# Kernel optimization log

Hardware: AMD Instinct MI355X
Metric: run time of the kernel (lower is better)

Reference implementation:

```python
import jax, jax.numpy as jnp
import numpy as np

NUM_HEADS = 16
HIDDEN = 1024
EPS = 1e-5


def _layer_norm(x, g, b):
    m = jnp.mean(x, axis=-1, keepdims=True)
    v = jnp.mean(jnp.square(x - m), axis=-1, keepdims=True)
    return (x - m) * jax.lax.rsqrt(v + EPS) * g + b


def setup_inputs() -> dict:
    key = jax.random.key(0)
    ks = jax.random.split(key, 6)
    B, S, H = 2, 2048, HIDDEN
    x = jax.random.normal(ks[0], (B, S, H), dtype=jnp.float32)
    # True = masked (original passes ~attn_mask to SDPA); causal mask
    causal = ~jnp.tril(jnp.ones((S, S), dtype=bool))
    attn_mask = causal[None, None, :, :]  # [1,1,S,S]
    sc = 1.0 / np.sqrt(H)
    qkv_w = jax.random.normal(ks[1], (H, 3 * H), dtype=jnp.float32) * sc
    qkv_b = jnp.zeros((3 * H,), dtype=jnp.float32)
    out_w = jax.random.normal(ks[2], (H, H), dtype=jnp.float32) * sc
    out_b = jnp.zeros((H,), dtype=jnp.float32)
    w1 = jax.random.normal(ks[3], (H, 4 * H), dtype=jnp.float32) * sc
    b1 = jnp.zeros((4 * H,), dtype=jnp.float32)
    w2 = jax.random.normal(ks[4], (4 * H, H), dtype=jnp.float32) * (1.0 / np.sqrt(4 * H))
    b2 = jnp.zeros((H,), dtype=jnp.float32)
    return {
        'x': x, 'attn_mask': attn_mask,
        'qkv_w': qkv_w, 'qkv_b': qkv_b, 'out_w': out_w, 'out_b': out_b,
        'w1': w1, 'b1': b1, 'w2': w2, 'b2': b2,
        'ln1_g': jnp.ones((H,), jnp.float32), 'ln1_b': jnp.zeros((H,), jnp.float32),
        'ln2_g': jnp.ones((H,), jnp.float32), 'ln2_b': jnp.zeros((H,), jnp.float32),
    }


def reference(x, attn_mask, qkv_w, qkv_b, out_w, out_b, w1, b1, w2, b2,
              ln1_g, ln1_b, ln2_g, ln2_b):
    B, S, H = x.shape
    nh = NUM_HEADS
    hd = H // nh
    qkv = x @ qkv_w + qkv_b                      # [B,S,3H]
    q, k, v = jnp.split(qkv, 3, axis=-1)
    q = q.reshape(B, S, nh, hd).transpose(0, 2, 1, 3)  # [B,nh,S,hd]
    k = k.reshape(B, S, nh, hd).transpose(0, 2, 1, 3)
    v = v.reshape(B, S, nh, hd).transpose(0, 2, 1, 3)
    scores = jnp.einsum('bhqd,bhkd->bhqk', q, k) / jnp.sqrt(jnp.asarray(hd, x.dtype))
    scores = jnp.where(attn_mask, jnp.finfo(scores.dtype).min, scores)
    p = jax.nn.softmax(scores, axis=-1)
    attn = jnp.einsum('bhqk,bhkd->bhqd', p, v)   # [B,nh,S,hd]
    attn = attn.transpose(0, 2, 1, 3).reshape(B, S, H)
    attn = attn @ out_w + out_b
    x = _layer_norm(x + attn, ln1_g, ln1_b)
    h = jax.nn.relu(x @ w1 + b1) @ w2 + b2
    x = _layer_norm(x + h, ln2_g, ln2_b)
    return x
```

## Files before the change

kernel.cpp:

```cpp
#include <hip/hip_runtime.h>
#include <hip/hip_bf16.h>

typedef __bf16 bf16x8 __attribute__((ext_vector_type(8)));
typedef __bf16 bf16x4 __attribute__((ext_vector_type(4)));
typedef float f32x4 __attribute__((ext_vector_type(4)));

__device__ __forceinline__ void gload16(void* lds, const void* g) {
  __builtin_amdgcn_global_load_lds((const __attribute__((address_space(1))) void*)g,
                                   (__attribute__((address_space(3))) void*)lds, 16, 0, 0);
}

__global__ __launch_bounds__(256)
void transpose_cast(const float* __restrict__ in, __bf16* __restrict__ out, int R, int C)
{
  __shared__ __bf16 tile[32][33];
  const int bc = blockIdx.x * 32, br = blockIdx.y * 32;
  const int lx = threadIdx.x & 31, ly = threadIdx.x >> 5;
#pragma unroll
  for (int p = 0; p < 4; ++p)
    tile[ly + p * 8][lx] = (__bf16)in[(size_t)(br + ly + p * 8) * C + bc + lx];
  __syncthreads();
#pragma unroll
  for (int p = 0; p < 4; ++p)
    out[(size_t)(bc + ly + p * 8) * R + br + lx] = tile[lx][ly + p * 8];
}

__global__ __launch_bounds__(256)
void vtrans(const __bf16* __restrict__ qkv, __bf16* __restrict__ vtg)
{
  __shared__ __bf16 tile[32][33];
  const int sx = blockIdx.x * 32;
  const int dy = blockIdx.y * 32;
  const int z = blockIdx.z;
  const int b = z >> 4, h = z & 15;
  const int lx = threadIdx.x & 31, ly = threadIdx.x >> 5;
  const __bf16* src = qkv + (size_t)b * 2048 * 3072 + 2048 + h * 64;
#pragma unroll
  for (int p = 0; p < 4; ++p)
    tile[ly + p * 8][lx] = src[(size_t)(sx + ly + p * 8) * 3072 + dy + lx];
  __syncthreads();
  __bf16* dst = vtg + (size_t)z * 64 * 2048;
#pragma unroll
  for (int p = 0; p < 4; ++p)
    dst[(size_t)(dy + ly + p * 8) * 2048 + sx + lx] = tile[lx][ly + p * 8];
}

__global__ __launch_bounds__(256)
void cast_bf16(const float* __restrict__ in, __bf16* __restrict__ out)
{
  const int i = (blockIdx.x * 256 + threadIdx.x) * 4;
  float4 v = *(const float4*)(in + i);
  out[i] = (__bf16)v.x; out[i + 1] = (__bf16)v.y;
  out[i + 2] = (__bf16)v.z; out[i + 3] = (__bf16)v.w;
}

template<int BN, bool OUT_BF16, bool RELU, bool RESID>
__global__ __launch_bounds__(256)
void gemm_bt(const __bf16* __restrict__ A, const __bf16* __restrict__ Bt,
             const float* __restrict__ bias, const float* __restrict__ resid,
             void* __restrict__ Cv, int M, int N, int K)
{
  constexpr int NW = BN / 32;
  __shared__ __bf16 As[2][128 * 64];
  __shared__ __bf16 Bs[2][BN * 64];
  const int tid = threadIdx.x;
  const int wave = tid >> 6, lane = tid & 63;
  const int g = lane >> 4, l16 = lane & 15;
  const int row0 = blockIdx.x * 128, col0 = blockIdx.y * BN;
  const int wr = wave >> 1, wc = wave & 1;
  f32x4 acc[4][NW] = {};
  const int nk = K >> 6;

  auto STAGE = [&](int buf, int k0) {
#pragma unroll
    for (int r = 0; r < 4; ++r) {
      const int seg = r * 256 + tid;
      const int arow = seg >> 3;
      const int ko = ((seg & 7) ^ (arow & 7)) * 8;
      gload16(&As[buf][(r * 256 + wave * 64) * 8], &A[(size_t)(row0 + arow) * K + k0 + ko]);
    }
#pragma unroll
    for (int r = 0; r < BN / 32; ++r) {
      const int seg = r * 256 + tid;
      const int brow = seg >> 3;
      const int ko = ((seg & 7) ^ (brow & 7)) * 8;
      gload16(&Bs[buf][(r * 256 + wave * 64) * 8], &Bt[(size_t)(col0 + brow) * K + k0 + ko]);
    }
  };

  STAGE(0, 0);
  __syncthreads();
  int cur = 0;
  for (int t = 0; t < nk; ++t) {
    if (t + 1 < nk) STAGE(cur ^ 1, (t + 1) << 6);
#pragma unroll
    for (int kk = 0; kk < 2; ++kk) {
      bf16x8 af[4], bfr[NW];
#pragma unroll
      for (int m = 0; m < 4; ++m) {
        const int row = wr * 64 + m * 16 + l16;
        af[m] = *(const bf16x8*)&As[cur][row * 64 + ((kk * 32 + g * 8) ^ ((row & 7) << 3))];
      }
#pragma unroll
      for (int n = 0; n < NW; ++n) {
        const int row = wc * (BN / 2) + n * 16 + l16;
        bfr[n] = *(const bf16x8*)&Bs[cur][row * 64 + ((kk * 32 + g * 8) ^ ((row & 7) << 3))];
      }
#pragma unroll
      for (int m = 0; m < 4; ++m)
#pragma unroll
        for (int n = 0; n < NW; ++n)
          acc[m][n] = __builtin_amdgcn_mfma_f32_16x16x32_bf16(af[m], bfr[n], acc[m][n], 0, 0, 0);
    }
    __syncthreads();
    cur ^= 1;
  }
#pragma unroll
  for (int n = 0; n < NW; ++n) {
    const int col = col0 + wc * (BN / 2) + n * 16 + l16;
    const float bv = bias[col];
#pragma unroll
    for (int m = 0; m < 4; ++m) {
      const int rrow = row0 + wr * 64 + m * 16 + g * 4;
#pragma unroll
      for (int r = 0; r < 4; ++r) {
        float v = acc[m][n][r] + bv;
        if (RESID) v += resid[(size_t)(rrow + r) * N + col];
        if (RELU)  v = fmaxf(v, 0.f);
        if (OUT_BF16) ((__bf16*)Cv)[(size_t)(rrow + r) * N + col] = (__bf16)v;
        else          ((float*)Cv)[(size_t)(rrow + r) * N + col] = v;
      }
    }
  }
}

template<bool RESID>
__global__ __launch_bounds__(256)
void gemm_splitk(const __bf16* __restrict__ A, const __bf16* __restrict__ Bt,
                 const float* __restrict__ bias, const float* __restrict__ resid,
                 float* __restrict__ C0, float* __restrict__ C1,
                 int M, int N, int Kfull, int Ksub)
{
  __shared__ __bf16 As[2][128 * 64];
  __shared__ __bf16 Bs[2][128 * 64];
  const int tid = threadIdx.x;
  const int wave = tid >> 6, lane = tid & 63;
  const int g = lane >> 4, l16 = lane & 15;
  const int row0 = blockIdx.x * 128, col0 = blockIdx.y * 128;
  const int z = blockIdx.z;
  const __bf16* Az = A + (size_t)z * Ksub;
  const __bf16* Bz = Bt + (size_t)z * Ksub;
  float* C = z ? C1 : C0;
  const int wr = wave >> 1, wc = wave & 1;
  f32x4 acc[4][4] = {};
  const int nk = Ksub >> 6;

  auto STAGE = [&](int buf, int k0) {
#pragma unroll
    for (int r = 0; r < 4; ++r) {
      const int seg = r * 256 + tid;
      const int arow = seg >> 3;
      const int ko = ((seg & 7) ^ (arow & 7)) * 8;
      gload16(&As[buf][(r * 256 + wave * 64) * 8], &Az[(size_t)(row0 + arow) * Kfull + k0 + ko]);
      gload16(&Bs[buf][(r * 256 + wave * 64) * 8], &Bz[(size_t)(col0 + arow) * Kfull + k0 + ko]);
    }
  };

  STAGE(0, 0);
  __syncthreads();
  int cur = 0;
  for (int t = 0; t < nk; ++t) {
    if (t + 1 < nk) STAGE(cur ^ 1, (t + 1) << 6);
#pragma unroll
    for (int kk = 0; kk < 2; ++kk) {
      bf16x8 af[4], bfr[4];
#pragma unroll
      for (int m = 0; m < 4; ++m) {
        const int row = wr * 64 + m * 16 + l16;
        af[m] = *(const bf16x8*)&As[cur][row * 64 + ((kk * 32 + g * 8) ^ ((row & 7) << 3))];
      }
#pragma unroll
      for (int n = 0; n < 4; ++n) {
        const int row = wc * 64 + n * 16 + l16;
        bfr[n] = *(const bf16x8*)&Bs[cur][row * 64 + ((kk * 32 + g * 8) ^ ((row & 7) << 3))];
      }
#pragma unroll
      for (int m = 0; m < 4; ++m)
#pragma unroll
        for (int n = 0; n < 4; ++n)
          acc[m][n] = __builtin_amdgcn_mfma_f32_16x16x32_bf16(af[m], bfr[n], acc[m][n], 0, 0, 0);
    }
    __syncthreads();
    cur ^= 1;
  }
#pragma unroll
  for (int n = 0; n < 4; ++n) {
    const int col = col0 + wc * 64 + n * 16 + l16;
    const float bv = (z == 0) ? bias[col] : 0.f;
#pragma unroll
    for (int m = 0; m < 4; ++m) {
      const int rrow = row0 + wr * 64 + m * 16 + g * 4;
#pragma unroll
      for (int r = 0; r < 4; ++r) {
        float v = acc[m][n][r] + bv;
        if (RESID) { if (z == 0) v += resid[(size_t)(rrow + r) * N + col]; }
        C[(size_t)(rrow + r) * N + col] = v;
      }
    }
  }
}

__global__ __launch_bounds__(256)
void attn_fwd(const __bf16* __restrict__ qkv, const __bf16* __restrict__ vtg,
              __bf16* __restrict__ ctx)
{
  constexpr int S = 2048, H = 1024, W3 = 3 * H;
  __shared__ __bf16 Ks[2][64 * 64];
  __shared__ __bf16 Vt[2][64 * 64];
  __shared__ __bf16 Ps[4][16 * 64];
  const int tid = threadIdx.x, wave = tid >> 6, lane = tid & 63;
  const int g = lane >> 4, l16 = lane & 15;
  const int perm = ((l16 & 7) << 1) | (l16 >> 3);
  const int bh = blockIdx.x;
  const int pr = blockIdx.y;
  const int b = bh >> 4, h = bh & 15;
  const size_t base = (size_t)b * S * W3;
  const __bf16* Qg = qkv + base;
  const __bf16* Kg = qkv + base + H;
  const __bf16* Vg = vtg + (size_t)bh * 64 * S;

  auto STAGE_KV = [&](int buf, int kv0) {
#pragma unroll
    for (int r = 0; r < 2; ++r) {
      const int seg = r * 256 + tid;
      const int row = seg >> 3;
      const int ko = ((seg & 7) ^ (row & 7)) * 8;
      gload16(&Ks[buf][(r * 256 + wave * 64) * 8], &Kg[(size_t)(kv0 + row) * W3 + h * 64 + ko]);
      gload16(&Vt[buf][(r * 256 + wave * 64) * 8], &Vg[(size_t)row * S + kv0 + ko]);
    }
  };

#pragma unroll 1
  for (int half = 0; half < 2; ++half) {
    const int qi = half ? (31 - blockIdx.y) : blockIdx.y;
    const int q0 = qi * 64;
    const int qrow = q0 + wave * 16 + l16;
    bf16x8 qa[2];
#pragma unroll
    for (int kk = 0; kk < 2; ++kk)
      qa[kk] = *(const bf16x8*)&Qg[(size_t)qrow * W3 + h * 64 + kk * 32 + g * 8];

    f32x4 o[4] = {};
    float lsum = 0.f;
    const int nT = qi + 1;

    STAGE_KV(0, 0);
    __syncthreads();
    int cur = 0;

    for (int t = 0; t < nT; ++t) {
      const int kv0 = t * 64;
      if (t + 1 < nT) STAGE_KV(cur ^ 1, kv0 + 64);

      f32x4 s[4] = {};
      __builtin_amdgcn_s_setprio(1);
#pragma unroll
      for (int kk = 0; kk < 2; ++kk) {
        bf16x8 kb[4];
#pragma unroll
        for (int n = 0; n < 4; ++n) {
          const int row = n * 16 + l16;
          kb[n] = *(const bf16x8*)&Ks[cur][row * 64 + ((kk * 32 + g * 8) ^ ((row & 7) << 3))];
        }
#pragma unroll
        for (int n = 0; n < 4; ++n)
          s[n] = __builtin_amdgcn_mfma_f32_16x16x32_bf16(kb[n], qa[kk], s[n], 0, 0, 0);
      }
      __builtin_amdgcn_s_setprio(0);

      const bool diag = (t == nT - 1);
#pragma unroll
      for (int n = 0; n < 4; ++n) {
        float lp[4];
#pragma unroll
        for (int r = 0; r < 4; ++r) {
          const int ka = kv0 + n * 16 + g * 4 + r;
          float p = exp2f(s[n][r] * 0.18033688f);
          if (diag && ka > qrow) p = 0.f;
          lp[r] = p;
          lsum += p;
        }
        bf16x4 pk;
        pk[0] = (__bf16)lp[0]; pk[1] = (__bf16)lp[1];
        pk[2] = (__bf16)lp[2]; pk[3] = (__bf16)lp[3];
        *(bf16x4*)&Ps[wave][l16 * 64 + (((4 * n + g) ^ perm) << 2)] = pk;
      }

      __builtin_amdgcn_s_setprio(1);
#pragma unroll
      for (int kk = 0; kk < 2; ++kk) {
        const int hb = 8 * kk + 2 * g;
        bf16x4 p0 = *(const bf16x4*)&Ps[wave][l16 * 64 + ((hb ^ perm) << 2)];
        bf16x4 p1 = *(const bf16x4*)&Ps[wave][l16 * 64 + (((hb + 1) ^ perm) << 2)];
        bf16x8 pa = __builtin_shufflevector(p0, p1, 0, 1, 2, 3, 4, 5, 6, 7);
        bf16x8 vb[4];
#pragma unroll
        for (int n2 = 0; n2 < 4; ++n2) {
          const int row = n2 * 16 + l16;
          vb[n2] = *(const bf16x8*)&Vt[cur][row * 64 + ((kk * 32 + g * 8) ^ ((row & 7) << 3))];
        }
#pragma unroll
        for (int n2 = 0; n2 < 4; ++n2)
          o[n2] = __builtin_amdgcn_mfma_f32_16x16x32_bf16(pa, vb[n2], o[n2], 0, 0, 0);
      }
      __builtin_amdgcn_s_setprio(0);
      __syncthreads();
      cur ^= 1;
    }

    lsum += __shfl_xor(lsum, 16);
    lsum += __shfl_xor(lsum, 32);
#pragma unroll
    for (int r = 0; r < 4; ++r) {
      const float den = __shfl(lsum, g * 4 + r);
      const float inv = 1.f / den;
      const int qr = q0 + wave * 16 + g * 4 + r;
#pragma unroll
      for (int n2 = 0; n2 < 4; ++n2) {
        const int d = n2 * 16 + l16;
        ctx[(size_t)(b * S + qr) * H + h * 64 + d] = (__bf16)(o[n2][r] * inv);
      }
    }
  }
}

template<bool WRITE_BF16, bool TWO_IN>
__global__ __launch_bounds__(256)
void ln_kernel(const float* __restrict__ in, const float* __restrict__ in2,
               const float* __restrict__ gw, const float* __restrict__ bw,
               float* __restrict__ outf, __bf16* __restrict__ outb)
{
  const int row = blockIdx.x, tid = threadIdx.x;
  float4 xv = ((const float4*)(in + (size_t)row * 1024))[tid];
  if (TWO_IN) {
    const float4 yv = ((const float4*)(in2 + (size_t)row * 1024))[tid];
    xv.x += yv.x; xv.y += yv.y; xv.z += yv.z; xv.w += yv.w;
  }
  float s = xv.x + xv.y + xv.z + xv.w;
  float s2 = xv.x * xv.x + xv.y * xv.y + xv.z * xv.z + xv.w * xv.w;
#pragma unroll
  for (int off = 32; off; off >>= 1) { s += __shfl_xor(s, off); s2 += __shfl_xor(s2, off); }
  __shared__ float ps[8];
  if ((tid & 63) == 0) { ps[tid >> 6] = s; ps[4 + (tid >> 6)] = s2; }
  __syncthreads();
  s = ps[0] + ps[1] + ps[2] + ps[3];
  s2 = ps[4] + ps[5] + ps[6] + ps[7];
  const float mean = s * (1.f / 1024.f);
  const float var = s2 * (1.f / 1024.f) - mean * mean;
  const float rs = rsqrtf(var + 1e-5f);
  const float4 gv = ((const float4*)gw)[tid];
  const float4 bv = ((const float4*)bw)[tid];
  float4 y;
  y.x = (xv.x - mean) * rs * gv.x + bv.x;
  y.y = (xv.y - mean) * rs * gv.y + bv.y;
  y.z = (xv.z - mean) * rs * gv.z + bv.z;
  y.w = (xv.w - mean) * rs * gv.w + bv.w;
  ((float4*)(outf + (size_t)row * 1024))[tid] = y;
  if (WRITE_BF16) {
    __bf16* ob = outb + (size_t)row * 1024 + tid * 4;
    ob[0] = (__bf16)y.x; ob[1] = (__bf16)y.y; ob[2] = (__bf16)y.z; ob[3] = (__bf16)y.w;
  }
}

extern "C" void kernel_launch(void* const* d_in, const int* in_sizes, int n_in,
                              void* d_out, int out_size, void* d_ws, size_t ws_size,
                              hipStream_t stream)
{
  (void)in_sizes; (void)n_in; (void)out_size; (void)ws_size;
  const float* x     = (const float*)d_in[0];
  const float* qkv_w = (const float*)d_in[2];
  const float* qkv_b = (const float*)d_in[3];
  const float* out_w = (const float*)d_in[4];
  const float* out_b = (const float*)d_in[5];
  const float* w1    = (const float*)d_in[6];
  const float* b1    = (const float*)d_in[7];
  const float* w2    = (const float*)d_in[8];
  const float* b2    = (const float*)d_in[9];
  const float* ln1g  = (const float*)d_in[10];
  const float* ln1b  = (const float*)d_in[11];
  const float* ln2g  = (const float*)d_in[12];
  const float* ln2b  = (const float*)d_in[13];

  char* ws = (char*)d_ws;
  __bf16* wt_qkv = (__bf16*)(ws + 0);
  __bf16* wt_out = (__bf16*)(ws + 6291456);
  __bf16* wt_w1  = (__bf16*)(ws + 8388608);
  __bf16* wt_w2  = (__bf16*)(ws + 16777216);
  __bf16* xb     = (__bf16*)(ws + 25165824);
  __bf16* big    = (__bf16*)(ws + 33554432);
  float*  res    = (float*)(ws + 67108864);
  float*  x1f    = (float*)(ws + 83886080);
  __bf16* x1b    = (__bf16*)(ws + 100663296);
  __bf16* vtg    = (__bf16*)res;
  float*  pB     = (float*)big;
  float*  qB     = (float*)ws;

  transpose_cast<<<dim3(96, 32), 256, 0, stream>>>(qkv_w, wt_qkv, 1024, 3072);
  transpose_cast<<<dim3(32, 32), 256, 0, stream>>>(out_w, wt_out, 1024, 1024);
  transpose_cast<<<dim3(128, 32), 256, 0, stream>>>(w1, wt_w1, 1024, 4096);
  transpose_cast<<<dim3(32, 128), 256, 0, stream>>>(w2, wt_w2, 4096, 1024);
  cast_bf16<<<4096, 256, 0, stream>>>(x, xb);

  gemm_bt<128, true, false, false><<<dim3(32, 24), 256, 0, stream>>>(xb, wt_qkv, qkv_b, nullptr, big, 4096, 3072, 1024);
  vtrans<<<dim3(64, 2, 32), 256, 0, stream>>>(big, vtg);
  attn_fwd<<<dim3(32, 16), 256, 0, stream>>>(big, vtg, xb);
  gemm_splitk<true><<<dim3(32, 8, 2), 256, 0, stream>>>(xb, wt_out, out_b, x, res, pB, 4096, 1024, 1024, 512);
  ln_kernel<true, true><<<4096, 256, 0, stream>>>(res, pB, ln1g, ln1b, x1f, x1b);
  gemm_bt<128, true, true, false><<<dim3(32, 32), 256, 0, stream>>>(x1b, wt_w1, b1, nullptr, big, 4096, 4096, 1024);
  gemm_splitk<true><<<dim3(32, 8, 2), 256, 0, stream>>>(big, wt_w2, b2, x1f, res, qB, 4096, 1024, 4096, 2048);
  ln_kernel<false, true><<<4096, 256, 0, stream>>>(res, qB, ln2g, ln2b, (float*)d_out, nullptr);
}
```

Baseline: 246.7 us.

## Add 256x256 eight-wave GEMM with interleaved prefetch and 4-way split-K FFN2

Introduces a 512-thread GEMM with 256x256 tiles that interleaves LDS staging of the next K-tiles with MFMA quarters, and uses it for the QKV and FFN1 projections. The FFN down projection becomes a 4-way split-K whose partials go into scratch buffers and are summed in a new fused four-input LayerNorm kernel. The out-projection switches from split-K to a single-pass gemm_bt with a fused residual. The aim is more data reuse per tile and better overlap of loads with compute. The cost is heavier register and LDS pressure and extra partial-sum traffic through reused workspace regions.

```diff
diff --git a/kernel.cpp b/kernel.cpp
--- a/kernel.cpp
+++ b/kernel.cpp
@@ -52,6 +52,151 @@
   float4 v = *(const float4*)(in + i);
   out[i] = (__bf16)v.x; out[i + 1] = (__bf16)v.y;
   out[i + 2] = (__bf16)v.z; out[i + 3] = (__bf16)v.w;
+}
+
+template<bool OUTBF16, bool RELU, bool SPLIT>
+__global__ __launch_bounds__(512, 2)
+void gemm256(const __bf16* __restrict__ A, const __bf16* __restrict__ Bt,
+             const float* __restrict__ bias,
+             void* __restrict__ C0v, float* __restrict__ P1,
+             float* __restrict__ P2lo, float* __restrict__ P2hi,
+             float* __restrict__ P3,
+             int M, int N, int Kfull, int Ksub)
+{
+  __shared__ __align__(16) __bf16 As[2][2][128 * 64];
+  __shared__ __align__(16) __bf16 Bs[2][2][128 * 64];
+  const int tid = threadIdx.x, wave = tid >> 6, lane = tid & 63;
+  const int g = lane >> 4, l16 = lane & 15;
+  const int wr = wave >> 2, wc = wave & 3;
+  const int row0 = blockIdx.x * 256, col0 = blockIdx.y * 256;
+  const int z = SPLIT ? blockIdx.z : 0;
+  const __bf16* Az = A + (size_t)z * Ksub;
+  const __bf16* Bz = Bt + (size_t)z * Ksub;
+  const int nk = Ksub >> 6;
+  f32x4 acc[8][4] = {};
+
+  auto SA = [&](int buf, int half, int kt) {
+    const int k0 = kt << 6;
+#pragma unroll
+    for (int r = 0; r < 2; ++r) {
+      const int seg = r * 512 + tid, rr = seg >> 3;
+      const int src = ((seg & 7) ^ (rr & 7)) << 3;
+      gload16(&As[buf][half][(size_t)(r * 512 + wave * 64) * 8],
+              &Az[(size_t)(row0 + half * 128 + rr) * Kfull + k0 + src]);
+    }
+  };
+  auto SB = [&](int buf, int half, int kt) {
+    const int k0 = kt << 6;
+#pragma unroll
+    for (int r = 0; r < 2; ++r) {
+      const int seg = r * 512 + tid, rr = seg >> 3;
+      const int src = ((seg & 7) ^ (rr & 7)) << 3;
+      gload16(&Bs[buf][half][(size_t)(r * 512 + wave * 64) * 8],
+              &Bz[(size_t)(col0 + half * 128 + rr) * Kfull + k0 + src]);
+    }
+  };
+
+  SA(0, 0, 0); SA(0, 1, 0); SB(0, 0, 0); SB(0, 1, 0);
+  { const int t1 = (nk > 1) ? 1 : 0; SB(1, 0, t1); SB(1, 1, t1); }
+  asm volatile("s_waitcnt vmcnt(4)" ::: "memory");
+  __builtin_amdgcn_sched_barrier(0);
+  __builtin_amdgcn_s_barrier();
+
+#pragma unroll 1
+  for (int t = 0; t < nk; ++t) {
+    const int p = t & 1;
+    const int tA = (t + 1 < nk) ? (t + 1) : (nk - 1);
+    const int tB = (t + 2 < nk) ? (t + 2) : (nk - 1);
+
+    bf16x8 bfr[4][2], af[2][2];
+
+#pragma unroll
+    for (int n = 0; n < 4; ++n) {
+      const int row = wc * 64 + n * 16 + l16;
+      const int hf = row >> 7, rr = row & 127;
+#pragma unroll
+      for (int ks = 0; ks < 2; ++ks)
+        bfr[n][ks] = *(const bf16x8*)&Bs[p][hf][rr * 64 + ((((ks << 2) + g) ^ (rr & 7)) << 3)];
+    }
+#pragma unroll
+    for (int m = 0; m < 2; ++m) {
+      const int rr = m * 16 + l16;
+#pragma unroll
+      for (int ks = 0; ks < 2; ++ks)
+        af[m][ks] = *(const bf16x8*)&As[p][wr][rr * 64 + ((((ks << 2) + g) ^ (rr & 7)) << 3)];
+    }
+    SA(p ^ 1, 0, tA);
+    __builtin_amdgcn_s_barrier();
+    asm volatile("s_waitcnt lgkmcnt(0)" ::: "memory");
+    __builtin_amdgcn_sched_barrier(0);
+    __builtin_amdgcn_s_setprio(1);
+#pragma unroll
+    for (int ks = 0; ks < 2; ++ks)
+#pragma unroll
+      for (int m = 0; m < 2; ++m)
+#pragma unroll
+        for (int n = 0; n < 4; ++n)
+          acc[m][n] = __builtin_amdgcn_mfma_f32_16x16x32_bf16(af[m][ks], bfr[n][ks], acc[m][n], 0, 0, 0);
+    __builtin_amdgcn_s_setprio(0);
+    __builtin_amdgcn_s_barrier();
+
+#pragma unroll
+    for (int q = 1; q < 4; ++q) {
+#pragma unroll
+      for (int m = 0; m < 2; ++m) {
+        const int rr = (2 * q + m) * 16 + l16;
+#pragma unroll
+        for (int ks = 0; ks < 2; ++ks)
+          af[m][ks] = *(const bf16x8*)&As[p][wr][rr * 64 + ((((ks << 2) + g) ^ (rr & 7)) << 3)];
+      }
+      if (q == 1)      SA(p ^ 1, 1, tA);
+      else if (q == 2) SB(p, 0, tB);
+      else             SB(p, 1, tB);
+      __builtin_amdgcn_s_barrier();
+      asm volatile("s_waitcnt lgkmcnt(0)" ::: "memory");
+      __builtin_amdgcn_sched_barrier(0);
+      __builtin_amdgcn_s_setprio(1);
+#pragma unroll
+      for (int ks = 0; ks < 2; ++ks)
+#pragma unroll
+        for (int m = 0; m < 2; ++m)
+#pragma unroll
+          for (int n = 0; n < 4; ++n)
+            acc[2 * q + m][n] = __builtin_amdgcn_mfma_f32_16x16x32_bf16(af[m][ks], bfr[n][ks], acc[2 * q + m][n], 0, 0, 0);
+      __builtin_amdgcn_s_setprio(0);
+      if (q == 3) {
+        asm volatile("s_waitcnt vmcnt(4)" ::: "memory");
+        __builtin_amdgcn_sched_barrier(0);
+      }
+      __builtin_amdgcn_s_barrier();
+    }
+  }
+
+#pragma unroll
+  for (int n = 0; n < 4; ++n) {
+    const int col = col0 + wc * 64 + n * 16 + l16;
+    float bv = 0.f;
+    if (!SPLIT || z == 0) bv = bias[col];
+#pragma unroll
+    for (int m = 0; m < 8; ++m) {
+      const int rbase = row0 + wr * 128 + m * 16 + g * 4;
+#pragma unroll
+      for (int j = 0; j < 4; ++j) {
+        float v = acc[m][n][j] + bv;
+        const size_t idx = (size_t)(rbase + j) * N + col;
+        if (SPLIT) {
+          if (z == 0)      ((float*)C0v)[idx] = v;
+          else if (z == 1) P1[idx] = v;
+          else if (z == 2) { float* C = (row0 < 2048) ? P2lo : P2hi; C[idx] = v; }
+          else             { v += P3[idx]; P3[idx] = v; }
+        } else {
+          if (RELU) v = fmaxf(v, 0.f);
+          if (OUTBF16) ((__bf16*)C0v)[idx] = (__bf16)v;
+          else         ((float*)C0v)[idx] = v;
+        }
+      }
+    }
+  }
 }
 
 template<int BN, bool OUT_BF16, bool RELU, bool RESID>
@@ -134,82 +279,6 @@
   }
 }
 
-template<bool RESID>
-__global__ __launch_bounds__(256)
-void gemm_splitk(const __bf16* __restrict__ A, const __bf16* __restrict__ Bt,
-                 const float* __restrict__ bias, const float* __restrict__ resid,
-                 float* __restrict__ C0, float* __restrict__ C1,
-                 int M, int N, int Kfull, int Ksub)
-{
-  __shared__ __bf16 As[2][128 * 64];
-  __shared__ __bf16 Bs[2][128 * 64];
-  const int tid = threadIdx.x;
-  const int wave = tid >> 6, lane = tid & 63;
-  const int g = lane >> 4, l16 = lane & 15;
-  const int row0 = blockIdx.x * 128, col0 = blockIdx.y * 128;
-  const int z = blockIdx.z;
-  const __bf16* Az = A + (size_t)z * Ksub;
-  const __bf16* Bz = Bt + (size_t)z * Ksub;
-  float* C = z ? C1 : C0;
-  const int wr = wave >> 1, wc = wave & 1;
-  f32x4 acc[4][4] = {};
-  const int nk = Ksub >> 6;
-
-  auto STAGE = [&](int buf, int k0) {
-#pragma unroll
-    for (int r = 0; r < 4; ++r) {
-      const int seg = r * 256 + tid;
-      const int arow = seg >> 3;
-      const int ko = ((seg & 7) ^ (arow & 7)) * 8;
-      gload16(&As[buf][(r * 256 + wave * 64) * 8], &Az[(size_t)(row0 + arow) * Kfull + k0 + ko]);
-      gload16(&Bs[buf][(r * 256 + wave * 64) * 8], &Bz[(size_t)(col0 + arow) * Kfull + k0 + ko]);
-    }
-  };
-
-  STAGE(0, 0);
-  __syncthreads();
-  int cur = 0;
-  for (int t = 0; t < nk; ++t) {
-    if (t + 1 < nk) STAGE(cur ^ 1, (t + 1) << 6);
-#pragma unroll
-    for (int kk = 0; kk < 2; ++kk) {
-      bf16x8 af[4], bfr[4];
-#pragma unroll
-      for (int m = 0; m < 4; ++m) {
-        const int row = wr * 64 + m * 16 + l16;
-        af[m] = *(const bf16x8*)&As[cur][row * 64 + ((kk * 32 + g * 8) ^ ((row & 7) << 3))];
-      }
-#pragma unroll
-      for (int n = 0; n < 4; ++n) {
-        const int row = wc * 64 + n * 16 + l16;
-        bfr[n] = *(const bf16x8*)&Bs[cur][row * 64 + ((kk * 32 + g * 8) ^ ((row & 7) << 3))];
-      }
-#pragma unroll
-      for (int m = 0; m < 4; ++m)
-#pragma unroll
-        for (int n = 0; n < 4; ++n)
-          acc[m][n] = __builtin_amdgcn_mfma_f32_16x16x32_bf16(af[m], bfr[n], acc[m][n], 0, 0, 0);
-    }
-    __syncthreads();
-    cur ^= 1;
-  }
-#pragma unroll
-  for (int n = 0; n < 4; ++n) {
-    const int col = col0 + wc * 64 + n * 16 + l16;
-    const float bv = (z == 0) ? bias[col] : 0.f;
-#pragma unroll
-    for (int m = 0; m < 4; ++m) {
-      const int rrow = row0 + wr * 64 + m * 16 + g * 4;
-#pragma unroll
-      for (int r = 0; r < 4; ++r) {
-        float v = acc[m][n][r] + bv;
-        if (RESID) { if (z == 0) v += resid[(size_t)(rrow + r) * N + col]; }
-        C[(size_t)(rrow + r) * N + col] = v;
-      }
-    }
-  }
-}
-
 __global__ __launch_bounds__(256)
 void attn_fwd(const __bf16* __restrict__ qkv, const __bf16* __restrict__ vtg,
               __bf16* __restrict__ ctx)
@@ -222,7 +291,6 @@
   const int g = lane >> 4, l16 = lane & 15;
   const int perm = ((l16 & 7) << 1) | (l16 >> 3);
   const int bh = blockIdx.x;
-  const int pr = blockIdx.y;
   const int b = bh >> 4, h = bh & 15;
   const size_t base = (size_t)b * S * W3;
   const __bf16* Qg = qkv + base;
@@ -372,6 +440,44 @@
   }
 }
 
+__global__ __launch_bounds__(256)
+void ln4_kernel(const float* __restrict__ in0, const float* __restrict__ in1,
+                const float* __restrict__ p2lo, const float* __restrict__ p2hi,
+                const float* __restrict__ in3,
+                const float* __restrict__ gw, const float* __restrict__ bw,
+                float* __restrict__ outf)
+{
+  const int row = blockIdx.x, tid = threadIdx.x;
+  const float* i2 = (row < 2048) ? p2lo : p2hi;
+  float4 a = ((const float4*)(in0 + (size_t)row * 1024))[tid];
+  float4 b = ((const float4*)(in1 + (size_t)row * 1024))[tid];
+  float4 c = ((const float4*)(i2  + (size_t)row * 1024))[tid];
+  float4 d = ((const float4*)(in3 + (size_t)row * 1024))[tid];
+  float4 xv;
+  xv.x = a.x + b.x + c.x + d.x; xv.y = a.y + b.y + c.y + d.y;
+  xv.z = a.z + b.z + c.z + d.z; xv.w = a.w + b.w + c.w + d.w;
+  float s = xv.x + xv.y + xv.z + xv.w;
+  float s2 = xv.x * xv.x + xv.y * xv.y + xv.z * xv.z + xv.w * xv.w;
+#pragma unroll
+  for (int off = 32; off; off >>= 1) { s += __shfl_xor(s, off); s2 += __shfl_xor(s2, off); }
+  __shared__ float ps[8];
+  if ((tid & 63) == 0) { ps[tid >> 6] = s; ps[4 + (tid >> 6)] = s2; }
+  __syncthreads();
+  s = ps[0] + ps[1] + ps[2] + ps[3];
+  s2 = ps[4] + ps[5] + ps[6] + ps[7];
+  const float mean = s * (1.f / 1024.f);
+  const float var = s2 * (1.f / 1024.f) - mean * mean;
+  const float rs = rsqrtf(var + 1e-5f);
+  const float4 gv = ((const float4*)gw)[tid];
+  const float4 bv = ((const float4*)bw)[tid];
+  float4 y;
+  y.x = (xv.x - mean) * rs * gv.x + bv.x;
+  y.y = (xv.y - mean) * rs * gv.y + bv.y;
+  y.z = (xv.z - mean) * rs * gv.z + bv.z;
+  y.w = (xv.w - mean) * rs * gv.w + bv.w;
+  ((float4*)(outf + (size_t)row * 1024))[tid] = y;
+}
+
 extern "C" void kernel_launch(void* const* d_in, const int* in_sizes, int n_in,
                               void* d_out, int out_size, void* d_ws, size_t ws_size,
                               hipStream_t stream)
@@ -402,8 +508,9 @@
   float*  x1f    = (float*)(ws + 83886080);
   __bf16* x1b    = (__bf16*)(ws + 100663296);
   __bf16* vtg    = (__bf16*)res;
-  float*  pB     = (float*)big;
-  float*  qB     = (float*)ws;
+  float*  P1     = (float*)ws;
+  float*  P2lo   = (float*)xb;
+  float*  P2hi   = (float*)x1b - (size_t)2048 * 1024;
 
   transpose_cast<<<dim3(96, 32), 256, 0, stream>>>(qkv_w, wt_qkv, 1024, 3072);
   transpose_cast<<<dim3(32, 32), 256, 0, stream>>>(out_w, wt_out, 1024, 1024);
@@ -411,12 +518,17 @@
   transpose_cast<<<dim3(32, 128), 256, 0, stream>>>(w2, wt_w2, 4096, 1024);
   cast_bf16<<<4096, 256, 0, stream>>>(x, xb);
 
-  gemm_bt<128, true, false, false><<<dim3(32, 24), 256, 0, stream>>>(xb, wt_qkv, qkv_b, nullptr, big, 4096, 3072, 1024);
+  gemm256<true, false, false><<<dim3(16, 12), 512, 0, stream>>>(
+      xb, wt_qkv, qkv_b, big, nullptr, nullptr, nullptr, nullptr, 4096, 3072, 1024, 1024);
   vtrans<<<dim3(64, 2, 32), 256, 0, stream>>>(big, vtg);
   attn_fwd<<<dim3(32, 16), 256, 0, stream>>>(big, vtg, xb);
-  gemm_splitk<true><<<dim3(32, 8, 2), 256, 0, stream>>>(xb, wt_out, out_b, x, res, pB, 4096, 1024, 1024, 512);
-  ln_kernel<true, true><<<4096, 256, 0, stream>>>(res, pB, ln1g, ln1b, x1f, x1b);
-  gemm_bt<128, true, true, false><<<dim3(32, 32), 256, 0, stream>>>(x1b, wt_w1, b1, nullptr, big, 4096, 4096, 1024);
-  gemm_splitk<true><<<dim3(32, 8, 2), 256, 0, stream>>>(big, wt_w2, b2, x1f, res, qB, 4096, 1024, 4096, 2048);
-  ln_kernel<false, true><<<4096, 256, 0, stream>>>(res, qB, ln2g, ln2b, (float*)d_out, nullptr);
-}
+  gemm_bt<64, false, false, true><<<dim3(32, 16), 256, 0, stream>>>(
+      xb, wt_out, out_b, x, res, 4096, 1024, 1024);
+  ln_kernel<true, false><<<4096, 256, 0, stream>>>(res, nullptr, ln1g, ln1b, x1f, x1b);
+  gemm256<true, true, false><<<dim3(16, 16), 512, 0, stream>>>(
+      x1b, wt_w1, b1, big, nullptr, nullptr, nullptr, nullptr, 4096, 4096, 1024, 1024);
+  gemm256<false, false, true><<<dim3(16, 4, 4), 512, 0, stream>>>(
+      big, wt_w2, b2, res, P1, P2lo, P2hi, x1f, 4096, 1024, 4096, 1024);
+  ln4_kernel<<<4096, 256, 0, stream>>>(res, P1, P2lo, P2hi, x1f, ln2g, ln2b,
+                                       (float*)d_out);
+}
```

Result: slower. 281.8 us (+14.2%).
